# Optimization experiments

Hardware: AMD Instinct MI355X
Metric: run time of the kernel (lower is better)

Reference implementation:

```python
import jax, jax.numpy as jnp
import numpy as np

B, S = 8, 2048

def setup_inputs() -> dict:
    key = jax.random.key(0)
    ks = iter(jax.random.split(key, 64))
    def lin(din, dout):
        w = jax.random.normal(next(ks), (din, dout), jnp.float32) / np.float32(np.sqrt(din))
        b = jax.random.normal(next(ks), (dout,), jnp.float32) * 0.01
        return w, b
    inp = {}
    inp['x'] = jax.random.normal(next(ks), (B, S, 256), jnp.float32)
    def blk(tag, d, ff):
        for name, (din, dout) in [('q',(d,d)),('k',(d,d)),('v',(d,d)),('o',(d,d)),('ff1',(d,ff)),('ff2',(ff,d))]:
            w, b = lin(din, dout)
            inp[f'{name}_w{tag}'] = w; inp[f'{name}_b{tag}'] = b
        inp[f'ln1_g{tag}'] = jnp.ones((d,), jnp.float32); inp[f'ln1_b{tag}'] = jnp.zeros((d,), jnp.float32)
        inp[f'ln2_g{tag}'] = jnp.ones((d,), jnp.float32); inp[f'ln2_b{tag}'] = jnp.zeros((d,), jnp.float32)
    blk(1, 256, 1024)
    blk(2, 128, 512)
    for nm, (din, dout) in [('dr1',(256,128)),('dr2',(128,64)),('dr3',(64,32)),('dr4',(32,14))]:
        w, b = lin(din, dout)
        inp[f'{nm}_w'] = w; inp[f'{nm}_b'] = b
    return inp

def _ln(x, g, b, eps=1e-5):
    m = x.mean(-1, keepdims=True)
    v = ((x - m) ** 2).mean(-1, keepdims=True)
    return (x - m) / jnp.sqrt(v + eps) * g + b

def _mha(x, wq, bq, wk, bk, wv, bv, wo, bo, h):
    Bx, Sx, D = x.shape
    hd = D // h
    q = (x @ wq + bq).reshape(Bx, Sx, h, hd).transpose(0, 2, 1, 3)
    k = (x @ wk + bk).reshape(Bx, Sx, h, hd).transpose(0, 2, 1, 3)
    v = (x @ wv + bv).reshape(Bx, Sx, h, hd).transpose(0, 2, 1, 3)
    scores = jnp.einsum('bhqd,bhkd->bhqk', q, k) / jnp.sqrt(jnp.float32(hd))  # [B,h,S,S]
    p = jax.nn.softmax(scores, axis=-1)
    o = jnp.einsum('bhqk,bhkd->bqhd', p, v).reshape(Bx, Sx, D)
    return o @ wo + bo

def _encoder(x, p, h):
    a = _mha(x, p['qw'], p['qb'], p['kw'], p['kb'], p['vw'], p['vb'], p['ow'], p['ob'], h)
    x = _ln(a + x, p['g1'], p['b1'])
    f = jax.nn.relu(x @ p['fw1'] + p['fb1']) @ p['fw2'] + p['fb2']
    return _ln(f + x, p['g2'], p['b2'])

def _pe(s, d):
    pos = jnp.arange(s, dtype=jnp.float32)[:, None]
    dep = jnp.arange(d, dtype=jnp.float32)[None, :]
    ang = pos / jnp.power(jnp.float32(10000.0), dep / d)
    even = (jnp.arange(d)[None, :] % 2) == 0
    return jnp.where(even, jnp.sin(ang), jnp.cos(ang))

def _forward(x,
             q_w1, q_b1, k_w1, k_b1, v_w1, v_b1, o_w1, o_b1,
             ff1_w1, ff1_b1, ff2_w1, ff2_b1, ln1_g1, ln1_b1, ln2_g1, ln2_b1,
             dr1_w, dr1_b,
             q_w2, q_b2, k_w2, k_b2, v_w2, v_b2, o_w2, o_b2,
             ff1_w2, ff1_b2, ff2_w2, ff2_b2, ln1_g2, ln1_b2, ln2_g2, ln2_b2,
             dr2_w, dr2_b, dr3_w, dr3_b, dr4_w, dr4_b):
    h = x + _pe(x.shape[1], x.shape[2])
    p1 = dict(qw=q_w1, qb=q_b1, kw=k_w1, kb=k_b1, vw=v_w1, vb=v_b1, ow=o_w1, ob=o_b1,
              fw1=ff1_w1, fb1=ff1_b1, fw2=ff2_w1, fb2=ff2_b1, g1=ln1_g1, b1=ln1_b1, g2=ln2_g1, b2=ln2_b1)
    h = _encoder(h, p1, 8)
    h = h @ dr1_w + dr1_b
    p2 = dict(qw=q_w2, qb=q_b2, kw=k_w2, kb=k_b2, vw=v_w2, vb=v_b2, ow=o_w2, ob=o_b2,
              fw1=ff1_w2, fb1=ff1_b2, fw2=ff2_w2, fb2=ff2_b2, g1=ln1_g2, b1=ln1_b2, g2=ln2_g2, b2=ln2_b2)
    h = _encoder(h, p2, 8)
    h = h @ dr2_w + dr2_b
    h = jnp.max(h, axis=1)  # AdaptiveMaxPool1d(1) over the sequence dim -> [B, 64]
    h = h @ dr3_w + dr3_b
    return h @ dr4_w + dr4_b  # [B, 14]

def reference(x,
              q_w1, q_b1, k_w1, k_b1, v_w1, v_b1, o_w1, o_b1,
              ff1_w1, ff1_b1, ff2_w1, ff2_b1, ln1_g1, ln1_b1, ln2_g1, ln2_b1,
              dr1_w, dr1_b,
              q_w2, q_b2, k_w2, k_b2, v_w2, v_b2, o_w2, o_b2,
              ff1_w2, ff1_b2, ff2_w2, ff2_b2, ln1_g2, ln1_b2, ln2_g2, ln2_b2,
              dr2_w, dr2_b, dr3_w, dr3_b, dr4_w, dr4_b):
    return _forward(x,
                    q_w1, q_b1, k_w1, k_b1, v_w1, v_b1, o_w1, o_b1,
                    ff1_w1, ff1_b1, ff2_w1, ff2_b1, ln1_g1, ln1_b1, ln2_g1, ln2_b1,
                    dr1_w, dr1_b,
                    q_w2, q_b2, k_w2, k_b2, v_w2, v_b2, o_w2, o_b2,
                    ff1_w2, ff1_b2, ff2_w2, ff2_b2, ln1_g2, ln1_b2, ln2_g2, ln2_b2,
                    dr2_w, dr2_b, dr3_w, dr3_b, dr4_w, dr4_b)
```

## Files before the change

### kernel.cpp

```cpp
#include <hip/hip_runtime.h>
#include <hip/hip_bf16.h>
#include <math.h>

#define SEQ  2048
#define BATCH 8
#define NTOK (SEQ*BATCH)

typedef __attribute__((ext_vector_type(8))) short short8v;
typedef __attribute__((ext_vector_type(4))) float f32x4;
typedef unsigned short u16;

__device__ __forceinline__ u16 f2bf(float f) {
    __hip_bfloat16 h = __float2bfloat16(f);
    return *reinterpret_cast<u16*>(&h);
}
__device__ __forceinline__ unsigned pack_bf2(float a, float b) {
    __hip_bfloat162 h = __float22bfloat162_rn(float2{a, b});
    return *reinterpret_cast<unsigned*>(&h);
}
__device__ __forceinline__ void gl_lds16(const u16* g, u16* l) {
    __builtin_amdgcn_global_load_lds(
        (const __attribute__((address_space(1))) unsigned int*)g,
        (__attribute__((address_space(3))) unsigned int*)l, 16, 0, 0);
}

struct WDescs {
    const float* src[14];
    int K[14];
    int N[14];
    long dst[14];
    float scale[14];
    int tstart[15];
};

__global__ __launch_bounds__(256) void convert_w_kernel(WDescs d, u16* __restrict__ WA) {
    __shared__ float tile[64][65];
    int blk = blockIdx.x;
    int di = 0;
    while (di < 13 && blk >= d.tstart[di + 1]) ++di;
    int t  = blk - d.tstart[di];
    int K  = d.K[di], N = d.N[di];
    int tn = N >> 6;
    int k0 = (t / tn) << 6, n0 = (t % tn) << 6;
    const float* src = d.src[di];
    float sc = d.scale[di];
    int tid = threadIdx.x;
    #pragma unroll
    for (int i = 0; i < 16; ++i) {
        int id = i * 256 + tid;
        int kk = id >> 6, nn = id & 63;
        tile[kk][nn] = src[(size_t)(k0 + kk) * N + n0 + nn];
    }
    __syncthreads();
    u16* dst = WA + d.dst[di];
    #pragma unroll
    for (int i = 0; i < 16; ++i) {
        int id = i * 256 + tid;
        int nn = id >> 6, kk = id & 63;
        dst[(size_t)(n0 + nn) * K + k0 + kk] = f2bf(tile[kk][nn] * sc);
    }
}

__global__ __launch_bounds__(256) void convert_bias_kernel(
    const float* qb1, const float* kb1, const float* vb1,
    const float* qb2, const float* kb2, const float* vb2,
    const float* dr2b, float* __restrict__ BA, float qs1, float qs2)
{
    int t = blockIdx.x * 256 + threadIdx.x;
    if      (t < 256)  BA[t] = qb1[t] * qs1;
    else if (t < 512)  BA[t] = kb1[t - 256];
    else if (t < 768)  BA[t] = vb1[t - 512];
    else if (t < 896)  BA[t] = qb2[t - 768] * qs2;
    else if (t < 1024) BA[t] = kb2[t - 896];
    else if (t < 1152) BA[t] = vb2[t - 1024];
    else if (t < 1216) BA[t] = dr2b[t - 1152];
    else if (t < 1280) BA[t] = 0.f;
}

__global__ __launch_bounds__(256) void add_pe_kernel(const float* __restrict__ x,
                                                     float* __restrict__ h,
                                                     u16* __restrict__ hb) {
    int idx = blockIdx.x * 256 + threadIdx.x;
    int s = idx >> 8;
    int d = idx & 255;
    float inv = exp2f((float)d * -0.0519051264732f);
    float ang = (float)s * inv;
    float pe  = (d & 1) ? __cosf(ang) : __sinf(ang);
    #pragma unroll
    for (int b = 0; b < BATCH; ++b) {
        size_t g = ((size_t)(b * SEQ + s) << 8) + d;
        float v = x[g] + pe;
        h[g]  = v;
        hb[g] = f2bf(v);
    }
}

template<int RELU, int WF32, int WBF16>
__global__ __launch_bounds__(256) void gemm_bf16_kernel(
    const u16* __restrict__ A, const u16* __restrict__ Bt,
    const float* __restrict__ bias, float* __restrict__ Cf,
    u16* __restrict__ Cb, int N, int K)
{
    __shared__ u16 As[128 * 64];
    __shared__ u16 Bs[128 * 64];
    const int tid  = threadIdx.x;
    const int lane = tid & 63;
    const int c    = lane & 15, g = lane >> 4;
    const int w    = tid >> 6;
    const int wr   = w >> 1, wc = w & 1;
    const size_t bm = (size_t)blockIdx.y * 128;
    const size_t bn = (size_t)blockIdx.x * 128;

    f32x4 acc[4][4];
    #pragma unroll
    for (int i = 0; i < 4; ++i)
        #pragma unroll
        for (int j = 0; j < 4; ++j) acc[i][j] = (f32x4){0.f, 0.f, 0.f, 0.f};

    const int nt = K >> 6;
    for (int t = 0; t < nt; ++t) {
        #pragma unroll
        for (int j = 0; j < 4; ++j) {
            int cid = j * 256 + tid;
            int row = cid >> 3, blk = cid & 7;
            int sof = (blk ^ (row & 7)) * 8;
            gl_lds16(&A [(bm + row) * K + t * 64 + sof], &As[cid * 8]);
            gl_lds16(&Bt[(bn + row) * K + t * 64 + sof], &Bs[cid * 8]);
        }
        __syncthreads();
        #pragma unroll
        for (int ks2 = 0; ks2 < 2; ++ks2) {
            short8v af[4], bfr[4];
            #pragma unroll
            for (int am = 0; am < 4; ++am) {
                int r = wr * 64 + am * 16 + c;
                af[am] = *(const short8v*)&As[r * 64 + (((ks2 * 4 + g) ^ (r & 7)) * 8)];
            }
            #pragma unroll
            for (int bn_ = 0; bn_ < 4; ++bn_) {
                int r = wc * 64 + bn_ * 16 + c;
                bfr[bn_] = *(const short8v*)&Bs[r * 64 + (((ks2 * 4 + g) ^ (r & 7)) * 8)];
            }
            #pragma unroll
            for (int am = 0; am < 4; ++am)
                #pragma unroll
                for (int bn_ = 0; bn_ < 4; ++bn_)
                    acc[am][bn_] = __builtin_amdgcn_mfma_f32_16x16x32_bf16(
                                       af[am], bfr[bn_], acc[am][bn_], 0, 0, 0);
        }
        __syncthreads();
    }

    float bv[4];
    #pragma unroll
    for (int bn_ = 0; bn_ < 4; ++bn_) bv[bn_] = bias[bn + wc * 64 + bn_ * 16 + c];
    #pragma unroll
    for (int am = 0; am < 4; ++am) {
        #pragma unroll
        for (int bn_ = 0; bn_ < 4; ++bn_) {
            #pragma unroll
            for (int i = 0; i < 4; ++i) {
                size_t row = bm + wr * 64 + am * 16 + 4 * g + i;
                size_t col = bn + wc * 64 + bn_ * 16 + c;
                float v = acc[am][bn_][i] + bv[bn_];
                if (RELU) v = fmaxf(v, 0.f);
                if (WF32)  Cf[row * N + col] = v;
                if (WBF16) Cb[row * N + col] = f2bf(v);
            }
        }
    }
}

template<int D, int WBF>
__global__ __launch_bounds__(256) void ln_residual_kernel(
    const float* __restrict__ a, const float* __restrict__ r,
    const float* __restrict__ g, const float* __restrict__ bb,
    float* __restrict__ out, u16* __restrict__ outb)
{
    const int N = D >> 6;
    int wave = threadIdx.x >> 6;
    int lane = threadIdx.x & 63;
    size_t token = (size_t)blockIdx.x * 4 + wave;
    const float* ar = a + token * D;
    const float* rr = r + token * D;

    float xv[N];
    float s = 0.f;
    #pragma unroll
    for (int i = 0; i < N; ++i) {
        int d = lane + (i << 6);
        xv[i] = ar[d] + rr[d];
        s += xv[i];
    }
    #pragma unroll
    for (int off = 1; off < 64; off <<= 1) s += __shfl_xor(s, off);
    float mean = s * (1.0f / D);
    float vs = 0.f;
    #pragma unroll
    for (int i = 0; i < N; ++i) { float d0 = xv[i] - mean; vs += d0 * d0; }
    #pragma unroll
    for (int off = 1; off < 64; off <<= 1) vs += __shfl_xor(vs, off);
    float inv = 1.0f / sqrtf(vs * (1.0f / D) + 1e-5f);
    #pragma unroll
    for (int i = 0; i < N; ++i) {
        int d = lane + (i << 6);
        float v = (xv[i] - mean) * inv * g[d] + bb[d];
        out[token * D + d] = v;
        if (WBF) outb[token * D + d] = f2bf(v);
    }
}

template<int HD>
__global__ __launch_bounds__(256) void flash_mfma_kernel(
    const u16* __restrict__ QKV, u16* __restrict__ Og)
{
    constexpr int D   = 8 * HD;
    constexpr int SD  = 3 * D;
    constexpr int NDH = HD / 16;

    __shared__ u16 Ks[2][64 * 32];
    __shared__ u16 Vt[2][NDH * 16 * 64];
    __shared__ u16 Pb[64 * 64];

    const int tid  = threadIdx.x;
    const int w    = tid >> 6;
    const int lane = tid & 63;
    const int c    = lane & 15;
    const int g    = lane >> 4;

    const int H    = blockIdx.x + (blockIdx.y << 4);
    const int bh   = H & 63;
    const int qblk = H >> 6;
    const int b = bh >> 3, hh = bh & 7;
    const size_t qvbase = (size_t)b * SEQ * SD + (size_t)hh * HD;
    const size_t obase  = (size_t)b * SEQ * D  + (size_t)hh * HD;
    const int qbase = qblk * 128;

    short8v qf[2];
    #pragma unroll
    for (int qb = 0; qb < 2; ++qb) {
        if (HD == 16 && g >= 2) {
            short8v z = {0, 0, 0, 0, 0, 0, 0, 0};
            qf[qb] = z;
        } else {
            int qrow = qbase + w * 32 + qb * 16 + c;
            qf[qb] = *(const short8v*)&QKV[qvbase + (size_t)qrow * SD + 8 * g];
        }
    }

    f32x4 oacc[2][NDH];
    float lreg[2][4];
    #pragma unroll
    for (int qb = 0; qb < 2; ++qb) {
        #pragma unroll
        for (int dh = 0; dh < NDH; ++dh) oacc[qb][dh] = (f32x4){0.f, 0.f, 0.f, 0.f};
        #pragma unroll
        for (int i = 0; i < 4; ++i) lreg[qb][i] = 0.f;
    }

    const int skey = tid >> 2;
    const int sch  = (tid & 3) * 8;
    const int spos = ((skey >> 5) << 5) + 2 * (skey & 15) + ((skey >> 4) & 1);
    const int squad = spos >> 3, soff = spos & 7;
    const bool vstager = !(HD == 16 && sch >= 16);
    const int vkc = (c & 7) ^ ((c & 8) >> 1);

    gl_lds16(&QKV[qvbase + (size_t)skey * SD + D + sch], &Ks[0][tid * 8]);
    if (vstager) {
        short8v v0 = *(const short8v*)&QKV[qvbase + (size_t)skey * SD + 2 * D + sch];
        #pragma unroll
        for (int i = 0; i < 8; ++i) {
            int row = sch + i;
            int vk = (row & 7) ^ ((row & 8) >> 1);
            Vt[0][row * 64 + ((squad ^ vk) << 3) + soff] = (u16)v0[i];
        }
    }
    __syncthreads();

    int buf = 0;
    const int NT = SEQ / 64;
    for (int t = 0; t < NT; ++t) {
        short8v vv = {0, 0, 0, 0, 0, 0, 0, 0};
        const bool pre = (t + 1 < NT);
        if (pre) {
            const size_t nb = qvbase + (size_t)((t + 1) * 64 + skey) * SD;
            if (vstager) vv = *(const short8v*)&QKV[nb + 2 * D + sch];
            gl_lds16(&QKV[nb + D + sch], &Ks[buf ^ 1][tid * 8]);
        }

        short8v kf[4];
        #pragma unroll
        for (int kh = 0; kh < 4; ++kh)
            kf[kh] = *(const short8v*)&Ks[buf][(16 * kh + c) * 32 + 8 * g];
        short8v vfr[NDH][2];
        #pragma unroll
        for (int dh = 0; dh < NDH; ++dh) {
            vfr[dh][0] = *(const short8v*)&Vt[buf][(16 * dh + c) * 64 + ((g ^ vkc) << 3)];
            vfr[dh][1] = *(const short8v*)&Vt[buf][(16 * dh + c) * 64 + (((4 + g) ^ vkc) << 3)];
        }

        #pragma unroll
        for (int qb = 0; qb < 2; ++qb) {
            f32x4 s[4];
            #pragma unroll
            for (int kh = 0; kh < 4; ++kh)
                s[kh] = __builtin_amdgcn_mfma_f32_16x16x32_bf16(
                            qf[qb], kf[kh], (f32x4){0.f, 0.f, 0.f, 0.f}, 0, 0, 0);

            #pragma unroll
            for (int i = 0; i < 4; ++i) {
                float p0 = exp2f(s[0][i]);
                float p1 = exp2f(s[1][i]);
                float p2 = exp2f(s[2][i]);
                float p3 = exp2f(s[3][i]);
                lreg[qb][i] += (p0 + p1) + (p2 + p3);
                int rr = 4 * g + i;
                int pk = (rr & 7) ^ ((rr & 8) >> 1);
                int base = (w * 16 + rr) * 64 + 2 * (c & 3);
                *(unsigned*)&Pb[base + (((c >> 2) ^ pk) << 3)]       = pack_bf2(p0, p1);
                *(unsigned*)&Pb[base + ((((c >> 2) + 4) ^ pk) << 3)] = pack_bf2(p2, p3);
            }

            short8v pf0 = *(const short8v*)&Pb[(w * 16 + c) * 64 + ((g ^ vkc) << 3)];
            short8v pf1 = *(const short8v*)&Pb[(w * 16 + c) * 64 + (((4 + g) ^ vkc) << 3)];
            #pragma unroll
            for (int dh = 0; dh < NDH; ++dh) {
                oacc[qb][dh] = __builtin_amdgcn_mfma_f32_16x16x32_bf16(
                                   pf0, vfr[dh][0], oacc[qb][dh], 0, 0, 0);
                oacc[qb][dh] = __builtin_amdgcn_mfma_f32_16x16x32_bf16(
                                   pf1, vfr[dh][1], oacc[qb][dh], 0, 0, 0);
            }
        }

        if (pre && vstager) {
            #pragma unroll
            for (int i = 0; i < 8; ++i) {
                int row = sch + i;
                int vk = (row & 7) ^ ((row & 8) >> 1);
                Vt[buf ^ 1][row * 64 + ((squad ^ vk) << 3) + soff] = (u16)vv[i];
            }
        }
        __syncthreads();
        buf ^= 1;
    }

    #pragma unroll
    for (int qb = 0; qb < 2; ++qb) {
        #pragma unroll
        for (int i = 0; i < 4; ++i) {
            float li = lreg[qb][i];
            li += __shfl_xor(li, 1);
            li += __shfl_xor(li, 2);
            li += __shfl_xor(li, 4);
            li += __shfl_xor(li, 8);
            float inv = 1.0f / li;
            int qrow = qbase + w * 32 + qb * 16 + 4 * g + i;
            #pragma unroll
            for (int dh = 0; dh < NDH; ++dh)
                Og[obase + (size_t)qrow * D + 16 * dh + c] = f2bf(oacc[qb][dh][i] * inv);
        }
    }
}

__global__ __launch_bounds__(256) void maxpool_kernel(const float* __restrict__ in,
                                                      float* __restrict__ out) {
    __shared__ float red[4][64];
    int b = blockIdx.x, d = threadIdx.x & 63, st = threadIdx.x >> 6;
    float m = -INFINITY;
    for (int s = st * (SEQ / 4); s < (st + 1) * (SEQ / 4); ++s)
        m = fmaxf(m, in[((size_t)b * SEQ + s) * 128 + d]);
    red[st][d] = m;
    __syncthreads();
    if (st == 0) {
        m = fmaxf(fmaxf(red[0][d], red[1][d]), fmaxf(red[2][d], red[3][d]));
        out[b * 64 + d] = m;
    }
}

__global__ __launch_bounds__(256) void head_kernel(
    const float* __restrict__ pooled,
    const float* __restrict__ w3, const float* __restrict__ b3,
    const float* __restrict__ w4, const float* __restrict__ b4,
    float* __restrict__ out)
{
    __shared__ float t[8][32];
    int tid = threadIdx.x;
    {
        int b = tid >> 5, j = tid & 31;
        float s = b3[j];
        #pragma unroll
        for (int k = 0; k < 64; ++k) s = fmaf(pooled[b * 64 + k], w3[k * 32 + j], s);
        t[b][j] = s;
    }
    __syncthreads();
    if (tid < 8 * 14) {
        int b = tid / 14, j = tid % 14;
        float s = b4[j];
        #pragma unroll
        for (int k = 0; k < 32; ++k) s = fmaf(t[b][k], w4[k * 14 + j], s);
        out[b * 14 + j] = s;
    }
}

extern "C" void kernel_launch(void* const* d_in, const int* in_sizes, int n_in,
                              void* d_out, int out_size, void* d_ws, size_t ws_size,
                              hipStream_t stream) {
    const float* x     = (const float*)d_in[0];
    const float* qw1   = (const float*)d_in[1];
    const float* qb1   = (const float*)d_in[2];
    const float* kw1   = (const float*)d_in[3];
    const float* kb1   = (const float*)d_in[4];
    const float* vw1   = (const float*)d_in[5];
    const float* vb1   = (const float*)d_in[6];
    const float* ow1   = (const float*)d_in[7];
    const float* ob1   = (const float*)d_in[8];
    const float* f1w1  = (const float*)d_in[9];
    const float* f1b1  = (const float*)d_in[10];
    const float* f2w1  = (const float*)d_in[11];
    const float* f2b1  = (const float*)d_in[12];
    const float* ln1g1 = (const float*)d_in[13];
    const float* ln1b1 = (const float*)d_in[14];
    const float* ln2g1 = (const float*)d_in[15];
    const float* ln2b1 = (const float*)d_in[16];
    const float* qw2   = (const float*)d_in[17];
    const float* qb2   = (const float*)d_in[18];
    const float* kw2   = (const float*)d_in[19];
    const float* kb2   = (const float*)d_in[20];
    const float* vw2   = (const float*)d_in[21];
    const float* vb2   = (const float*)d_in[22];
    const float* ow2   = (const float*)d_in[23];
    const float* ob2   = (const float*)d_in[24];
    const float* f1w2  = (const float*)d_in[25];
    const float* f1b2  = (const float*)d_in[26];
    const float* f2w2  = (const float*)d_in[27];
    const float* f2b2  = (const float*)d_in[28];
    const float* ln1g2 = (const float*)d_in[29];
    const float* ln1b2 = (const float*)d_in[30];
    const float* ln2g2 = (const float*)d_in[31];
    const float* ln2b2 = (const float*)d_in[32];
    const float* dr1w  = (const float*)d_in[33];
    const float* dr1b  = (const float*)d_in[34];
    const float* dr2w  = (const float*)d_in[35];
    const float* dr2b  = (const float*)d_in[36];
    const float* dr3w  = (const float*)d_in[37];
    const float* dr3b  = (const float*)d_in[38];
    const float* dr4w  = (const float*)d_in[39];
    const float* dr4b  = (const float*)d_in[40];

    const size_t T = NTOK;
    float* F1 = (float*)d_ws;
    float* F2 = F1 + T * 256;
    u16*   E1 = (u16*)(F2 + T * 256);
    u16*   E2 = E1 + T * 256;
    u16*   E3 = E2 + T * 256;
    u16*   Dq = E3 + T * 256;
    u16*   WA = Dq + T * 1024;
    float* BA = (float*)(WA + 1048576);

    const float QS1 = 0.25503488f;
    const float QS2 = 0.36067376f;

    WDescs wd;
    const float* srcs[14] = {qw1, kw1, vw1, ow1, f1w1, f2w1, dr1w,
                             qw2, kw2, vw2, ow2, f1w2, f2w2, dr2w};
    int Ks_[14]  = {256, 256, 256, 256, 256, 1024, 256, 128, 128, 128, 128, 128, 512, 128};
    int Ns_[14]  = {256, 256, 256, 256, 1024, 256, 128, 128, 128, 128, 128, 512, 128, 64};
    long dsts[14] = {0, 65536, 131072, 196608, 262144, 524288, 786432,
                     819200, 835584, 851968, 868352, 884736, 950272, 1015808};
    float scs[14] = {QS1, 1.f, 1.f, 1.f, 1.f, 1.f, 1.f, QS2, 1.f, 1.f, 1.f, 1.f, 1.f, 1.f};
    int tst[15] = {0, 16, 32, 48, 64, 128, 192, 200, 204, 208, 212, 216, 232, 248, 250};
    for (int i = 0; i < 14; ++i) {
        wd.src[i] = srcs[i]; wd.K[i] = Ks_[i]; wd.N[i] = Ns_[i];
        wd.dst[i] = dsts[i]; wd.scale[i] = scs[i];
    }
    for (int i = 0; i < 15; ++i) wd.tstart[i] = tst[i];

    const dim3 blk(256);

    convert_w_kernel<<<250, blk, 0, stream>>>(wd, WA);
    convert_bias_kernel<<<5, blk, 0, stream>>>(qb1, kb1, vb1, qb2, kb2, vb2, dr2b, BA, QS1, QS2);

    add_pe_kernel<<<SEQ, blk, 0, stream>>>(x, F1, E1);

    gemm_bf16_kernel<0,0,1><<<dim3(6, 128), blk, 0, stream>>>(E1, WA + 0,      BA,   nullptr, Dq, 768, 256);
    flash_mfma_kernel<32><<<dim3(16, 64), blk, 0, stream>>>(Dq, E2);
    gemm_bf16_kernel<0,1,0><<<dim3(2, 128), blk, 0, stream>>>(E2, WA + 196608, ob1,  F2, nullptr, 256, 256);
    ln_residual_kernel<256,1><<<NTOK / 4, blk, 0, stream>>>(F2, F1, ln1g1, ln1b1, F1, E1);
    gemm_bf16_kernel<1,0,1><<<dim3(8, 128), blk, 0, stream>>>(E1, WA + 262144, f1b1, nullptr, Dq, 1024, 256);
    gemm_bf16_kernel<0,1,0><<<dim3(2, 128), blk, 0, stream>>>(Dq, WA + 524288, f2b1, F2, nullptr, 256, 1024);
    ln_residual_kernel<256,1><<<NTOK / 4, blk, 0, stream>>>(F2, F1, ln2g1, ln2b1, F1, E1);

    gemm_bf16_kernel<0,1,1><<<dim3(1, 128), blk, 0, stream>>>(E1, WA + 786432, dr1b, F2, E2, 128, 256);

    gemm_bf16_kernel<0,0,1><<<dim3(3, 128), blk, 0, stream>>>(E2, WA + 819200, BA + 768, nullptr, Dq, 384, 128);
    flash_mfma_kernel<16><<<dim3(16, 64), blk, 0, stream>>>(Dq, E3);
    gemm_bf16_kernel<0,1,0><<<dim3(1, 128), blk, 0, stream>>>(E3, WA + 868352, ob2,  F1, nullptr, 128, 128);
    ln_residual_kernel<128,1><<<NTOK / 4, blk, 0, stream>>>(F1, F2, ln1g2, ln1b2, F2, E1);
    gemm_bf16_kernel<1,0,1><<<dim3(4, 128), blk, 0, stream>>>(E1, WA + 884736, f1b2, nullptr, Dq, 512, 128);
    gemm_bf16_kernel<0,1,0><<<dim3(1, 128), blk, 0, stream>>>(Dq, WA + 950272, f2b2, F1, nullptr, 128, 512);
    ln_residual_kernel<128,1><<<NTOK / 4, blk, 0, stream>>>(F1, F2, ln2g2, ln2b2, F2, E1);

    gemm_bf16_kernel<0,1,0><<<dim3(1, 128), blk, 0, stream>>>(E1, WA + 1015808, BA + 1152, F1, nullptr, 128, 128);
    maxpool_kernel<<<BATCH, blk, 0, stream>>>(F1, F2);
    head_kernel<<<1, blk, 0, stream>>>(F2, dr3w, dr3b, dr4w, dr4b, (float*)d_out);
}
```

Baseline: 603.6 us.

## Use 8-wave flash attention blocks and narrower GEMM tiles for small-N layers

The flash attention kernel now runs 512 threads per block, with each wave owning 16 query rows instead of 32. K and V staging move onto separate thread halves, and K is stored in LDS with an XOR swizzle. Unused head-dim lanes for HD=16 load from a shared zero buffer. The GEMM kernel gains a BN template parameter so the N=128/384 layers use 128x64 tiles and launch more blocks. This trades more waves and more parallelism for less per-thread register state and some extra K/V reloads per block, and it assumes the zero-source buffer really holds zeros.

```diff
diff --git a/kernel.cpp b/kernel.cpp
--- a/kernel.cpp
+++ b/kernel.cpp
@@ -95,27 +95,28 @@
     }
 }
 
-template<int RELU, int WF32, int WBF16>
+template<int BN, int RELU, int WF32, int WBF16>
 __global__ __launch_bounds__(256) void gemm_bf16_kernel(
     const u16* __restrict__ A, const u16* __restrict__ Bt,
     const float* __restrict__ bias, float* __restrict__ Cf,
     u16* __restrict__ Cb, int N, int K)
 {
+    constexpr int NBF = BN / 32;
     __shared__ u16 As[128 * 64];
-    __shared__ u16 Bs[128 * 64];
+    __shared__ u16 Bs[BN * 64];
     const int tid  = threadIdx.x;
     const int lane = tid & 63;
     const int c    = lane & 15, g = lane >> 4;
     const int w    = tid >> 6;
     const int wr   = w >> 1, wc = w & 1;
     const size_t bm = (size_t)blockIdx.y * 128;
-    const size_t bn = (size_t)blockIdx.x * 128;
-
-    f32x4 acc[4][4];
+    const size_t bn = (size_t)blockIdx.x * BN;
+
+    f32x4 acc[4][NBF];
     #pragma unroll
     for (int i = 0; i < 4; ++i)
         #pragma unroll
-        for (int j = 0; j < 4; ++j) acc[i][j] = (f32x4){0.f, 0.f, 0.f, 0.f};
+        for (int j = 0; j < NBF; ++j) acc[i][j] = (f32x4){0.f, 0.f, 0.f, 0.f};
 
     const int nt = K >> 6;
     for (int t = 0; t < nt; ++t) {
@@ -124,44 +125,50 @@
             int cid = j * 256 + tid;
             int row = cid >> 3, blk = cid & 7;
             int sof = (blk ^ (row & 7)) * 8;
-            gl_lds16(&A [(bm + row) * K + t * 64 + sof], &As[cid * 8]);
+            gl_lds16(&A[(bm + row) * K + t * 64 + sof], &As[cid * 8]);
+        }
+        #pragma unroll
+        for (int j = 0; j < NBF; ++j) {
+            int cid = j * 256 + tid;
+            int row = cid >> 3, blk = cid & 7;
+            int sof = (blk ^ (row & 7)) * 8;
             gl_lds16(&Bt[(bn + row) * K + t * 64 + sof], &Bs[cid * 8]);
         }
         __syncthreads();
         #pragma unroll
         for (int ks2 = 0; ks2 < 2; ++ks2) {
-            short8v af[4], bfr[4];
+            short8v af[4], bfr[NBF];
             #pragma unroll
             for (int am = 0; am < 4; ++am) {
                 int r = wr * 64 + am * 16 + c;
                 af[am] = *(const short8v*)&As[r * 64 + (((ks2 * 4 + g) ^ (r & 7)) * 8)];
             }
             #pragma unroll
-            for (int bn_ = 0; bn_ < 4; ++bn_) {
-                int r = wc * 64 + bn_ * 16 + c;
+            for (int bn_ = 0; bn_ < NBF; ++bn_) {
+                int r = wc * (BN / 2) + bn_ * 16 + c;
                 bfr[bn_] = *(const short8v*)&Bs[r * 64 + (((ks2 * 4 + g) ^ (r & 7)) * 8)];
             }
             #pragma unroll
             for (int am = 0; am < 4; ++am)
                 #pragma unroll
-                for (int bn_ = 0; bn_ < 4; ++bn_)
+                for (int bn_ = 0; bn_ < NBF; ++bn_)
                     acc[am][bn_] = __builtin_amdgcn_mfma_f32_16x16x32_bf16(
                                        af[am], bfr[bn_], acc[am][bn_], 0, 0, 0);
         }
         __syncthreads();
     }
 
-    float bv[4];
-    #pragma unroll
-    for (int bn_ = 0; bn_ < 4; ++bn_) bv[bn_] = bias[bn + wc * 64 + bn_ * 16 + c];
+    float bv[NBF];
+    #pragma unroll
+    for (int bn_ = 0; bn_ < NBF; ++bn_) bv[bn_] = bias[bn + wc * (BN / 2) + bn_ * 16 + c];
     #pragma unroll
     for (int am = 0; am < 4; ++am) {
         #pragma unroll
-        for (int bn_ = 0; bn_ < 4; ++bn_) {
+        for (int bn_ = 0; bn_ < NBF; ++bn_) {
             #pragma unroll
             for (int i = 0; i < 4; ++i) {
                 size_t row = bm + wr * 64 + am * 16 + 4 * g + i;
-                size_t col = bn + wc * 64 + bn_ * 16 + c;
+                size_t col = bn + wc * (BN / 2) + bn_ * 16 + c;
                 float v = acc[am][bn_][i] + bv[bn_];
                 if (RELU) v = fmaxf(v, 0.f);
                 if (WF32)  Cf[row * N + col] = v;
@@ -211,8 +218,8 @@
 }
 
 template<int HD>
-__global__ __launch_bounds__(256) void flash_mfma_kernel(
-    const u16* __restrict__ QKV, u16* __restrict__ Og)
+__global__ __launch_bounds__(512) void flash_mfma_kernel(
+    const u16* __restrict__ QKV, u16* __restrict__ Og, const u16* __restrict__ zsrc)
 {
     constexpr int D   = 8 * HD;
     constexpr int SD  = 3 * D;
@@ -220,7 +227,7 @@
 
     __shared__ u16 Ks[2][64 * 32];
     __shared__ u16 Vt[2][NDH * 16 * 64];
-    __shared__ u16 Pb[64 * 64];
+    __shared__ u16 Pb[128 * 64];
 
     const int tid  = threadIdx.x;
     const int w    = tid >> 6;
@@ -236,36 +243,38 @@
     const size_t obase  = (size_t)b * SEQ * D  + (size_t)hh * HD;
     const int qbase = qblk * 128;
 
-    short8v qf[2];
-    #pragma unroll
-    for (int qb = 0; qb < 2; ++qb) {
-        if (HD == 16 && g >= 2) {
-            short8v z = {0, 0, 0, 0, 0, 0, 0, 0};
-            qf[qb] = z;
-        } else {
-            int qrow = qbase + w * 32 + qb * 16 + c;
-            qf[qb] = *(const short8v*)&QKV[qvbase + (size_t)qrow * SD + 8 * g];
-        }
-    }
-
-    f32x4 oacc[2][NDH];
-    float lreg[2][4];
-    #pragma unroll
-    for (int qb = 0; qb < 2; ++qb) {
-        #pragma unroll
-        for (int dh = 0; dh < NDH; ++dh) oacc[qb][dh] = (f32x4){0.f, 0.f, 0.f, 0.f};
-        #pragma unroll
-        for (int i = 0; i < 4; ++i) lreg[qb][i] = 0.f;
-    }
-
-    const int skey = tid >> 2;
-    const int sch  = (tid & 3) * 8;
-    const int spos = ((skey >> 5) << 5) + 2 * (skey & 15) + ((skey >> 4) & 1);
+    short8v qf;
+    if (HD == 16 && g >= 2) {
+        short8v z = {0, 0, 0, 0, 0, 0, 0, 0};
+        qf = z;
+    } else {
+        int qrow = qbase + w * 16 + c;
+        qf = *(const short8v*)&QKV[qvbase + (size_t)qrow * SD + 8 * g];
+    }
+
+    f32x4 oacc[NDH];
+    float lreg[4];
+    #pragma unroll
+    for (int dh = 0; dh < NDH; ++dh) oacc[dh] = (f32x4){0.f, 0.f, 0.f, 0.f};
+    #pragma unroll
+    for (int i = 0; i < 4; ++i) lreg[i] = 0.f;
+
+    const bool kstager = (tid < 256);
+    const int krow = tid >> 2;
+    const int klb  = (tid & 3) ^ ((krow >> 1) & 3);
+    const bool kzero = (HD == 16) && (klb >= 2);
+
+    const int vtid = tid - 256;
+    const int skey = vtid >> 2;
+    const int sch  = (vtid & 3) * 8;
+    const bool vstager = (tid >= 256) && (HD == 32 || sch < 16);
+    const int spos  = ((skey >> 5) << 5) + 2 * (skey & 15) + ((skey >> 4) & 1);
     const int squad = spos >> 3, soff = spos & 7;
-    const bool vstager = !(HD == 16 && sch >= 16);
     const int vkc = (c & 7) ^ ((c & 8) >> 1);
 
-    gl_lds16(&QKV[qvbase + (size_t)skey * SD + D + sch], &Ks[0][tid * 8]);
+    if (kstager)
+        gl_lds16(kzero ? zsrc : &QKV[qvbase + (size_t)krow * SD + D + klb * 8],
+                 &Ks[0][tid * 8]);
     if (vstager) {
         short8v v0 = *(const short8v*)&QKV[qvbase + (size_t)skey * SD + 2 * D + sch];
         #pragma unroll
@@ -283,15 +292,20 @@
         short8v vv = {0, 0, 0, 0, 0, 0, 0, 0};
         const bool pre = (t + 1 < NT);
         if (pre) {
-            const size_t nb = qvbase + (size_t)((t + 1) * 64 + skey) * SD;
-            if (vstager) vv = *(const short8v*)&QKV[nb + 2 * D + sch];
-            gl_lds16(&QKV[nb + D + sch], &Ks[buf ^ 1][tid * 8]);
+            if (kstager)
+                gl_lds16(kzero ? zsrc
+                               : &QKV[qvbase + (size_t)((t + 1) * 64 + krow) * SD + D + klb * 8],
+                         &Ks[buf ^ 1][tid * 8]);
+            if (vstager)
+                vv = *(const short8v*)&QKV[qvbase + (size_t)((t + 1) * 64 + skey) * SD + 2 * D + sch];
         }
 
         short8v kf[4];
         #pragma unroll
-        for (int kh = 0; kh < 4; ++kh)
-            kf[kh] = *(const short8v*)&Ks[buf][(16 * kh + c) * 32 + 8 * g];
+        for (int kh = 0; kh < 4; ++kh) {
+            int row = 16 * kh + c;
+            kf[kh] = *(const short8v*)&Ks[buf][row * 32 + ((g ^ ((c >> 1) & 3)) * 8)];
+        }
         short8v vfr[NDH][2];
         #pragma unroll
         for (int dh = 0; dh < NDH; ++dh) {
@@ -299,37 +313,32 @@
             vfr[dh][1] = *(const short8v*)&Vt[buf][(16 * dh + c) * 64 + (((4 + g) ^ vkc) << 3)];
         }
 
-        #pragma unroll
-        for (int qb = 0; qb < 2; ++qb) {
-            f32x4 s[4];
-            #pragma unroll
-            for (int kh = 0; kh < 4; ++kh)
-                s[kh] = __builtin_amdgcn_mfma_f32_16x16x32_bf16(
-                            qf[qb], kf[kh], (f32x4){0.f, 0.f, 0.f, 0.f}, 0, 0, 0);
-
-            #pragma unroll
-            for (int i = 0; i < 4; ++i) {
-                float p0 = exp2f(s[0][i]);
-                float p1 = exp2f(s[1][i]);
-                float p2 = exp2f(s[2][i]);
-                float p3 = exp2f(s[3][i]);
-                lreg[qb][i] += (p0 + p1) + (p2 + p3);
-                int rr = 4 * g + i;
-                int pk = (rr & 7) ^ ((rr & 8) >> 1);
-                int base = (w * 16 + rr) * 64 + 2 * (c & 3);
-                *(unsigned*)&Pb[base + (((c >> 2) ^ pk) << 3)]       = pack_bf2(p0, p1);
-                *(unsigned*)&Pb[base + ((((c >> 2) + 4) ^ pk) << 3)] = pack_bf2(p2, p3);
-            }
-
-            short8v pf0 = *(const short8v*)&Pb[(w * 16 + c) * 64 + ((g ^ vkc) << 3)];
-            short8v pf1 = *(const short8v*)&Pb[(w * 16 + c) * 64 + (((4 + g) ^ vkc) << 3)];
-            #pragma unroll
-            for (int dh = 0; dh < NDH; ++dh) {
-                oacc[qb][dh] = __builtin_amdgcn_mfma_f32_16x16x32_bf16(
-                                   pf0, vfr[dh][0], oacc[qb][dh], 0, 0, 0);
-                oacc[qb][dh] = __builtin_amdgcn_mfma_f32_16x16x32_bf16(
-                                   pf1, vfr[dh][1], oacc[qb][dh], 0, 0, 0);
-            }
+        f32x4 s[4];
+        #pragma unroll
+        for (int kh = 0; kh < 4; ++kh)
+            s[kh] = __builtin_amdgcn_mfma_f32_16x16x32_bf16(
+                        qf, kf[kh], (f32x4){0.f, 0.f, 0.f, 0.f}, 0, 0, 0);
+
+        #pragma unroll
+        for (int i = 0; i < 4; ++i) {
+            float p0 = exp2f(s[0][i]);
+            float p1 = exp2f(s[1][i]);
+            float p2 = exp2f(s[2][i]);
+            float p3 = exp2f(s[3][i]);
+            lreg[i] += (p0 + p1) + (p2 + p3);
+            int rr = 4 * g + i;
+            int pk = (rr & 7) ^ ((rr & 8) >> 1);
+            int base = (w * 16 + rr) * 64 + 2 * (c & 3);
+            *(unsigned*)&Pb[base + (((c >> 2) ^ pk) << 3)]       = pack_bf2(p0, p1);
+            *(unsigned*)&Pb[base + ((((c >> 2) + 4) ^ pk) << 3)] = pack_bf2(p2, p3);
+        }
+
+        short8v pf0 = *(const short8v*)&Pb[(w * 16 + c) * 64 + ((g ^ vkc) << 3)];
+        short8v pf1 = *(const short8v*)&Pb[(w * 16 + c) * 64 + (((4 + g) ^ vkc) << 3)];
+        #pragma unroll
+        for (int dh = 0; dh < NDH; ++dh) {
+            oacc[dh] = __builtin_amdgcn_mfma_f32_16x16x32_bf16(pf0, vfr[dh][0], oacc[dh], 0, 0, 0);
+            oacc[dh] = __builtin_amdgcn_mfma_f32_16x16x32_bf16(pf1, vfr[dh][1], oacc[dh], 0, 0, 0);
         }
 
         if (pre && vstager) {
@@ -345,20 +354,17 @@
     }
 
     #pragma unroll
-    for (int qb = 0; qb < 2; ++qb) {
-        #pragma unroll
-        for (int i = 0; i < 4; ++i) {
-            float li = lreg[qb][i];
-            li += __shfl_xor(li, 1);
-            li += __shfl_xor(li, 2);
-            li += __shfl_xor(li, 4);
-            li += __shfl_xor(li, 8);
-            float inv = 1.0f / li;
-            int qrow = qbase + w * 32 + qb * 16 + 4 * g + i;
-            #pragma unroll
-            for (int dh = 0; dh < NDH; ++dh)
-                Og[obase + (size_t)qrow * D + 16 * dh + c] = f2bf(oacc[qb][dh][i] * inv);
-        }
+    for (int i = 0; i < 4; ++i) {
+        float li = lreg[i];
+        li += __shfl_xor(li, 1);
+        li += __shfl_xor(li, 2);
+        li += __shfl_xor(li, 4);
+        li += __shfl_xor(li, 8);
+        float inv = 1.0f / li;
+        int qrow = qbase + w * 16 + 4 * g + i;
+        #pragma unroll
+        for (int dh = 0; dh < NDH; ++dh)
+            Og[obase + (size_t)qrow * D + 16 * dh + c] = f2bf(oacc[dh][i] * inv);
     }
 }
 
@@ -456,6 +462,7 @@
     u16*   Dq = E3 + T * 256;
     u16*   WA = Dq + T * 1024;
     float* BA = (float*)(WA + 1048576);
+    const u16* ZS = (const u16*)(BA + 1216);
 
     const float QS1 = 0.25503488f;
     const float QS2 = 0.36067376f;
@@ -476,31 +483,32 @@
     for (int i = 0; i < 15; ++i) wd.tstart[i] = tst[i];
 
     const dim3 blk(256);
+    const dim3 blk512(512);
 
     convert_w_kernel<<<250, blk, 0, stream>>>(wd, WA);
     convert_bias_kernel<<<5, blk, 0, stream>>>(qb1, kb1, vb1, qb2, kb2, vb2, dr2b, BA, QS1, QS2);
 
     add_pe_kernel<<<SEQ, blk, 0, stream>>>(x, F1, E1);
 
-    gemm_bf16_kernel<0,0,1><<<dim3(6, 128), blk, 0, stream>>>(E1, WA + 0,      BA,   nullptr, Dq, 768, 256);
-    flash_mfma_kernel<32><<<dim3(16, 64), blk, 0, stream>>>(Dq, E2);
-    gemm_bf16_kernel<0,1,0><<<dim3(2, 128), blk, 0, stream>>>(E2, WA + 196608, ob1,  F2, nullptr, 256, 256);
+    gemm_bf16_kernel<128,0,0,1><<<dim3(6, 128), blk, 0, stream>>>(E1, WA + 0,      BA,   nullptr, Dq, 768, 256);
+    flash_mfma_kernel<32><<<dim3(16, 64), blk512, 0, stream>>>(Dq, E2, ZS);
+    gemm_bf16_kernel<128,0,1,0><<<dim3(2, 128), blk, 0, stream>>>(E2, WA + 196608, ob1,  F2, nullptr, 256, 256);
     ln_residual_kernel<256,1><<<NTOK / 4, blk, 0, stream>>>(F2, F1, ln1g1, ln1b1, F1, E1);
-    gemm_bf16_kernel<1,0,1><<<dim3(8, 128), blk, 0, stream>>>(E1, WA + 262144, f1b1, nullptr, Dq, 1024, 256);
-    gemm_bf16_kernel<0,1,0><<<dim3(2, 128), blk, 0, stream>>>(Dq, WA + 524288, f2b1, F2, nullptr, 256, 1024);
+    gemm_bf16_kernel<128,1,0,1><<<dim3(8, 128), blk, 0, stream>>>(E1, WA + 262144, f1b1, nullptr, Dq, 1024, 256);
+    gemm_bf16_kernel<128,0,1,0><<<dim3(2, 128), blk, 0, stream>>>(Dq, WA + 524288, f2b1, F2, nullptr, 256, 1024);
     ln_residual_kernel<256,1><<<NTOK / 4, blk, 0, stream>>>(F2, F1, ln2g1, ln2b1, F1, E1);
 
-    gemm_bf16_kernel<0,1,1><<<dim3(1, 128), blk, 0, stream>>>(E1, WA + 786432, dr1b, F2, E2, 128, 256);
-
-    gemm_bf16_kernel<0,0,1><<<dim3(3, 128), blk, 0, stream>>>(E2, WA + 819200, BA + 768, nullptr, Dq, 384, 128);
-    flash_mfma_kernel<16><<<dim3(16, 64), blk, 0, stream>>>(Dq, E3);
-    gemm_bf16_kernel<0,1,0><<<dim3(1, 128), blk, 0, stream>>>(E3, WA + 868352, ob2,  F1, nullptr, 128, 128);
+    gemm_bf16_kernel<64,0,1,1><<<dim3(2, 128), blk, 0, stream>>>(E1, WA + 786432, dr1b, F2, E2, 128, 256);
+
+    gemm_bf16_kernel<64,0,0,1><<<dim3(6, 128), blk, 0, stream>>>(E2, WA + 819200, BA + 768, nullptr, Dq, 384, 128);
+    flash_mfma_kernel<16><<<dim3(16, 64), blk512, 0, stream>>>(Dq, E3, ZS);
+    gemm_bf16_kernel<64,0,1,0><<<dim3(2, 128), blk, 0, stream>>>(E3, WA + 868352, ob2,  F1, nullptr, 128, 128);
     ln_residual_kernel<128,1><<<NTOK / 4, blk, 0, stream>>>(F1, F2, ln1g2, ln1b2, F2, E1);
-    gemm_bf16_kernel<1,0,1><<<dim3(4, 128), blk, 0, stream>>>(E1, WA + 884736, f1b2, nullptr, Dq, 512, 128);
-    gemm_bf16_kernel<0,1,0><<<dim3(1, 128), blk, 0, stream>>>(Dq, WA + 950272, f2b2, F1, nullptr, 128, 512);
+    gemm_bf16_kernel<128,1,0,1><<<dim3(4, 128), blk, 0, stream>>>(E1, WA + 884736, f1b2, nullptr, Dq, 512, 128);
+    gemm_bf16_kernel<64,0,1,0><<<dim3(2, 128), blk, 0, stream>>>(Dq, WA + 950272, f2b2, F1, nullptr, 128, 512);
     ln_residual_kernel<128,1><<<NTOK / 4, blk, 0, stream>>>(F1, F2, ln2g2, ln2b2, F2, E1);
 
-    gemm_bf16_kernel<0,1,0><<<dim3(1, 128), blk, 0, stream>>>(E1, WA + 1015808, BA + 1152, F1, nullptr, 128, 128);
+    gemm_bf16_kernel<64,0,1,0><<<dim3(2, 128), blk, 0, stream>>>(E1, WA + 1015808, BA + 1152, F1, nullptr, 128, 128);
     maxpool_kernel<<<BATCH, blk, 0, stream>>>(F1, F2);
     head_kernel<<<1, blk, 0, stream>>>(F2, dr3w, dr3b, dr4w, dr4b, (float*)d_out);
 }
```

Measured after the change: 605.9 us. Within noise of the previous version (+0.4%).
